# Performance work log

Measured on AMD Instinct MI355X. Metric: run time of the kernel, lower is better.

Reference implementation:

```python
import jax, jax.numpy as jnp
import numpy as np

P_SIZES = (1, 2, 4)
O_SIZE = 32
EPS = 1e-5


def bilin_matrix(S, O):
    """Interpolation matrix (O, S) for torch UpsamplingBilinear2d (align_corners=True)."""
    if S == 1:
        return jnp.ones((O, 1), dtype=jnp.float32)
    pos = jnp.arange(O, dtype=jnp.float32) * ((S - 1) / (O - 1))
    lo = jnp.clip(jnp.floor(pos).astype(jnp.int32), 0, S - 2)
    frac = pos - lo.astype(jnp.float32)
    rows = jnp.arange(O)
    M = jnp.zeros((O, S), dtype=jnp.float32)
    M = M.at[rows, lo].add(1.0 - frac).at[rows, lo + 1].add(frac)
    return M


def setup_inputs() -> dict:
    key = jax.random.key(0)
    ks = jax.random.split(key, 12)
    n, C, H = 16, 512, 32
    c4 = C // 4      # 128, value/pyramid channels
    qk = c4 // 8     # 16, query/key channels inside SAE
    s = 0.05
    return {
        "x": jax.random.normal(ks[0], (n, C, H, H), jnp.float32),
        "rce_w": jax.random.normal(ks[1], (3, c4, C), jnp.float32) * s,   # 1x1 conv per pyramid scale
        "rce_b": jax.random.normal(ks[2], (3, c4), jnp.float32) * s,
        "q_w": jax.random.normal(ks[3], (qk, c4), jnp.float32) * s,       # SAE query 1x1 conv
        "q_b": jax.random.normal(ks[4], (qk,), jnp.float32) * s,
        "k_w": jax.random.normal(ks[5], (qk, c4), jnp.float32) * s,       # SAE key 1x1 conv
        "k_b": jax.random.normal(ks[6], (qk,), jnp.float32) * s,
        "value_w": jax.random.normal(ks[7], (c4, C), jnp.float32) * s,    # value 1x1 conv
        "value_b": jax.random.normal(ks[8], (c4,), jnp.float32) * s,
        "fusion_w": jax.random.normal(ks[9], (C, 3 * c4, 3, 3), jnp.float32) * s,  # 3x3 conv, no bias
        "bn_scale": 1.0 + jax.random.normal(ks[10], (C,), jnp.float32) * s,
        "bn_bias": jax.random.normal(ks[11], (C,), jnp.float32) * s,
        "gamma": jnp.asarray(0.5, jnp.float32),
    }


def reference(x, rce_w, rce_b, q_w, q_b, k_w, k_b, value_w, value_b,
              fusion_w, bn_scale, bn_bias, gamma):
    n, C, H, W = x.shape
    c4 = C // 4
    L = H * W

    # value projection: 1x1 conv then flatten -> (n, c4, L)
    proj_value = (jnp.einsum('oc,nchw->nohw', value_w, x)
                  + value_b[None, :, None, None]).reshape(n, c4, L)

    outs = []
    for i, sz in enumerate(P_SIZES):
        # AdaptiveAvgPool2d((sz, sz)) with divisible input -> exact uniform pooling
        pooled = x.reshape(n, C, sz, H // sz, sz, W // sz).mean(axis=(3, 5))
        # 1x1 conv C -> c4
        feat = jnp.einsum('oc,ncij->noij', rce_w[i], pooled) + rce_b[i][None, :, None, None]
        # bilinear upsample (align_corners=True) to (O_SIZE, O_SIZE)
        M = bilin_matrix(sz, O_SIZE)
        up = jnp.einsum('oi,pj,ncij->ncop', M, M, feat)  # (n, c4, H, W)
        # SAE: query/key 1x1 convs, flatten, bmm + softmax
        q = (jnp.einsum('oc,nchw->nohw', q_w, up) + q_b[None, :, None, None]).reshape(n, -1, L)
        k = (jnp.einsum('oc,nchw->nohw', k_w, up) + k_b[None, :, None, None]).reshape(n, -1, L)
        energy = jnp.einsum('ncl,ncm->nlm', q, k)        # (n, L, L)
        attn = jax.nn.softmax(energy, axis=-1)
        # temp = bmm(value, attn^T): temp[c,m] = sum_l value[c,l] * attn[m,l]
        outs.append(jnp.einsum('ncl,nml->ncm', proj_value, attn).reshape(n, c4, H, W))

    cat = jnp.concatenate(outs, axis=1)                  # (n, 3*c4, H, W)
    y = jax.lax.conv_general_dilated(
        cat, fusion_w, window_strides=(1, 1), padding=((1, 1), (1, 1)),
        dimension_numbers=('NCHW', 'OIHW', 'NCHW'))
    # BatchNorm2d in training mode (default): batch statistics over (N, H, W)
    mean = y.mean(axis=(0, 2, 3))
    var = y.var(axis=(0, 2, 3))
    y = (y - mean[None, :, None, None]) * (bn_scale / jnp.sqrt(var + EPS))[None, :, None, None] \
        + bn_bias[None, :, None, None]
    y = jax.nn.relu(y)
    return gamma * y + x
```

## Files before the change

### kernel.cpp

```cpp
#include <hip/hip_runtime.h>
#include <hip/hip_fp16.h>
#include <math.h>

#define OFF_COR   0u
#define OFF_PVH   2097152u
#define OFF_Y     3145728u
#define OFF_CATP  11534336u
#define OFF_QH    15085568u
#define OFF_KH    15347712u
#define OFF_POOL  16134144u
#define OFF_FEAT  16297984u
#define OFF_AW    16338944u
#define OFF_MEANS 17223680u
#define OFF_STAT  17225728u
#define OFF_VWH   17226752u

typedef __bf16 bf16x8 __attribute__((ext_vector_type(8)));
typedef _Float16 f16x8 __attribute__((ext_vector_type(8)));
typedef _Float16 f16x4 __attribute__((ext_vector_type(4)));
typedef float f32x4 __attribute__((ext_vector_type(4)));

__device__ __forceinline__ unsigned short f2bf(float f) {
  unsigned int u = __float_as_uint(f);
  unsigned int r = u + 0x7fff + ((u >> 16) & 1);
  return (unsigned short)(r >> 16);
}

__device__ __forceinline__ unsigned short f2h(float f) {
  union { _Float16 h; unsigned short u; } cv;
  cv.h = (_Float16)f;
  return cv.u;
}

__device__ __forceinline__ void gload_lds16(const void* g, void* l) {
  __builtin_amdgcn_global_load_lds(
      (const __attribute__((address_space(1))) unsigned int*)g,
      (__attribute__((address_space(3))) unsigned int*)l, 16, 0, 0);
}

__global__ __launch_bounds__(256) void pool_kernel(const float* __restrict__ x,
                                                   float* __restrict__ pool) {
  int b = blockIdx.x;
  int t = threadIdx.x;
  const float4* xp = (const float4*)(x + (size_t)b * 1024);
  float4 v = xp[t];
  float s4 = v.x + v.y + v.z + v.w;
  __shared__ float sm[256];
  __shared__ float p4s[16];
  sm[t] = s4;
  __syncthreads();
  if (t < 16) {
    int br = t >> 2, bc = t & 3;
    float s = 0.f;
#pragma unroll
    for (int rr = 0; rr < 8; ++rr) {
      int base = br * 64 + rr * 8 + bc * 2;
      s += sm[base] + sm[base + 1];
    }
    s *= (1.f / 64.f);
    p4s[t] = s;
    pool[(size_t)b * 20 + t] = s;
  }
  __syncthreads();
  if (t < 4) {
    int i2 = t >> 1, j2 = t & 1;
    float s = (p4s[(2*i2)*4 + 2*j2]     + p4s[(2*i2)*4 + 2*j2 + 1] +
               p4s[(2*i2+1)*4 + 2*j2]   + p4s[(2*i2+1)*4 + 2*j2 + 1]) * 0.25f;
    pool[(size_t)b * 20 + 16 + t] = s;
  }
}

__global__ __launch_bounds__(64) void feat_kernel(const float* __restrict__ pool,
                                                  const float* __restrict__ rce_w,
                                                  const float* __restrict__ rce_b,
                                                  float* __restrict__ feat) {
  int o = blockIdx.x, n = blockIdx.y, t = threadIdx.x;
  float part[20];
#pragma unroll
  for (int j = 0; j < 20; ++j) part[j] = 0.f;
  for (int c = t; c < 512; c += 64) {
    const float* pl = pool + ((size_t)n * 512 + c) * 20;
    float w2 = rce_w[(size_t)(128 + o) * 512 + c];
    float w4 = rce_w[(size_t)(256 + o) * 512 + c];
#pragma unroll
    for (int j = 0; j < 4; ++j)  part[j]     += w2 * pl[16 + j];
#pragma unroll
    for (int j = 0; j < 16; ++j) part[4 + j] += w4 * pl[j];
  }
  __shared__ float red[64][20];
#pragma unroll
  for (int j = 0; j < 20; ++j) red[t][j] = part[j];
  __syncthreads();
  if (t < 20) {
    float s = 0.f;
    for (int i = 0; i < 64; ++i) s += red[i][t];
    s += (t < 4) ? rce_b[128 + o] : rce_b[256 + o];
    feat[((size_t)n * 128 + o) * 20 + t] = s;
  }
}

__global__ __launch_bounds__(256) void qk2_kernel(const float* __restrict__ feat,
                                                  const float* __restrict__ q_w,
                                                  const float* __restrict__ q_b,
                                                  const float* __restrict__ k_w,
                                                  const float* __restrict__ k_b,
                                                  unsigned short* __restrict__ qh,
                                                  unsigned short* __restrict__ kh) {
  int n = blockIdx.x, t = threadIdx.x;
  __shared__ float fL[128 * 20];
  __shared__ float GH[2][16][20];
  for (int idx = t; idx < 2560; idx += 256) fL[idx] = feat[(size_t)n * 2560 + idx];
  __syncthreads();
  for (int idx = t; idx < 640; idx += 256) {
    int which = idx / 320, rem = idx % 320, qc = rem / 20, j = rem % 20;
    const float* w = which ? k_w : q_w;
    float s = which ? k_b[qc] : q_b[qc];
    for (int c = 0; c < 128; ++c) s += w[qc * 128 + c] * fL[c * 20 + j];
    GH[which][qc][j] = s;
  }
  __syncthreads();
  for (int it = blockIdx.y * 2; it < blockIdx.y * 2 + 2; ++it) {
    int row = t + 256 * it;
    int l = row & 1023, which = (row >> 10) & 1, s = row >> 11;
    int ry = l >> 5, cx = l & 31;
    int t0, t1, t2, t3;
    float w0, w1, w2, w3;
    if (s == 0) {
      float a = ry * (1.0f / 31.0f), b = cx * (1.0f / 31.0f);
      t0 = 0; t1 = 1; t2 = 2; t3 = 3;
      w0 = (1.f - a) * (1.f - b); w1 = (1.f - a) * b;
      w2 = a * (1.f - b);         w3 = a * b;
    } else {
      float pr = ry * (3.0f / 31.0f);
      int lr = (int)pr; if (lr > 2) lr = 2;
      float fr = pr - (float)lr;
      float pc = cx * (3.0f / 31.0f);
      int lc = (int)pc; if (lc > 2) lc = 2;
      float fc = pc - (float)lc;
      int base = 4 + lr * 4 + lc;
      t0 = base; t1 = base + 1; t2 = base + 4; t3 = base + 5;
      w0 = (1.f - fr) * (1.f - fc); w1 = (1.f - fr) * fc;
      w2 = fr * (1.f - fc);         w3 = fr * fc;
    }
    float val[16];
#pragma unroll
    for (int qc = 0; qc < 16; ++qc) {
      const float* G = GH[which][qc];
      val[qc] = w0 * G[t0] + w1 * G[t1] + w2 * G[t2] + w3 * G[t3];
    }
    unsigned short* dst = (which ? kh : qh) + (((size_t)(s * 16 + n) * 1024 + l) * 16);
#pragma unroll
    for (int u = 0; u < 4; ++u)
      *(ushort4*)(dst + 4 * u) = make_ushort4(f2h(val[4*u]), f2h(val[4*u+1]),
                                              f2h(val[4*u+2]), f2h(val[4*u+3]));
  }
}

__global__ __launch_bounds__(256) void xcast_kernel(const float* __restrict__ x,
                                                    unsigned short* __restrict__ xT) {
  int lt = blockIdx.x, ct = blockIdx.y, n = blockIdx.z;
  int l0 = lt * 64, c0 = ct * 64, t = threadIdx.x;
  __shared__ float tile[64 * 65];
#pragma unroll
  for (int i = 0; i < 16; ++i) {
    int idx = t + 256 * i;
    int c = idx >> 6, l = idx & 63;
    tile[c * 65 + l] = x[((size_t)n * 512 + c0 + c) * 1024 + l0 + l];
  }
  __syncthreads();
#pragma unroll
  for (int i = 0; i < 16; ++i) {
    int idx = t + 256 * i;
    int l = idx >> 6, c = idx & 63;
    xT[((size_t)n * 1024 + l0 + l) * 512 + c0 + c] = f2h(tile[c * 65 + l]);
  }
}

__global__ __launch_bounds__(256) void vwcast_kernel(const float* __restrict__ vw,
                                                     unsigned short* __restrict__ vwh) {
  int i = blockIdx.x * 256 + threadIdx.x;
  vwh[i] = f2h(vw[i]);
}

__global__ __launch_bounds__(256) void pvmm2_kernel(const unsigned short* __restrict__ vwh,
                                                    const unsigned short* __restrict__ xT,
                                                    const float* __restrict__ vb,
                                                    unsigned short* __restrict__ pvh) {
  int l0 = blockIdx.x * 64;
  int n = blockIdx.y;
  int t = threadIdx.x, lane = t & 63, wv = t >> 6;
  int wm = (wv & 1) * 64, wn = (wv >> 1) * 32;

  __shared__ short Asm[128 * 32];
  __shared__ short Bsm[64 * 32];

  int ar0 = t >> 2,        aq0 = (t & 3) ^ ((ar0 >> 1) & 3);
  int idx1 = t + 256; int ar1 = idx1 >> 2, aq1 = (idx1 & 3) ^ ((ar1 >> 1) & 3);
  int br  = t >> 2,        bq  = (t & 3) ^ ((br >> 1) & 3);
  const unsigned short* Ab0 = vwh + (size_t)ar0 * 512 + aq0 * 8;
  const unsigned short* Ab1 = vwh + (size_t)ar1 * 512 + aq1 * 8;
  const unsigned short* Bb  = xT + ((size_t)n * 1024 + l0 + br) * 512 + bq * 8;
  char* ldsA = (char*)Asm;
  char* ldsB = (char*)Bsm;
  int wvoff = wv * 1024;
  int r15 = lane & 15, kg = lane >> 4;
  int kq = kg ^ ((r15 >> 1) & 3);

  f32x4 acc[4][2];
#pragma unroll
  for (int i = 0; i < 4; ++i)
#pragma unroll
    for (int j = 0; j < 2; ++j) acc[i][j] = (f32x4){0.f, 0.f, 0.f, 0.f};

  for (int k0 = 0; k0 < 512; k0 += 32) {
    __syncthreads();
    gload_lds16(Ab0 + k0, ldsA + wvoff);
    gload_lds16(Ab1 + k0, ldsA + 4096 + wvoff);
    gload_lds16(Bb + k0,  ldsB + wvoff);
    __syncthreads();
    f16x8 af[4], bfr[2];
#pragma unroll
    for (int mt2 = 0; mt2 < 4; ++mt2)
      af[mt2] = *(const f16x8*)&Asm[(wm + mt2 * 16 + r15) * 32 + kq * 8];
#pragma unroll
    for (int nt2 = 0; nt2 < 2; ++nt2)
      bfr[nt2] = *(const f16x8*)&Bsm[(wn + nt2 * 16 + r15) * 32 + kq * 8];
#pragma unroll
    for (int mt2 = 0; mt2 < 4; ++mt2)
#pragma unroll
      for (int nt2 = 0; nt2 < 2; ++nt2)
        acc[mt2][nt2] = __builtin_amdgcn_mfma_f32_16x16x32_f16(af[mt2], bfr[nt2], acc[mt2][nt2], 0, 0, 0);
  }

  int c_lo = wm + (lane >> 4) * 4;
  int l_lo = wn + (lane & 15);
#pragma unroll
  for (int mt2 = 0; mt2 < 4; ++mt2)
#pragma unroll
    for (int nt2 = 0; nt2 < 2; ++nt2) {
      int l = l0 + l_lo + nt2 * 16;
#pragma unroll
      for (int r = 0; r < 4; ++r) {
        int c = c_lo + mt2 * 16 + r;
        pvh[((size_t)n * 128 + c) * 1024 + l] = f2h(acc[mt2][nt2][r] + vb[c]);
      }
    }
}

__global__ __launch_bounds__(256) void mean_kernel(const unsigned short* __restrict__ pvh,
                                                   float* __restrict__ means) {
  int c = blockIdx.x, n = blockIdx.y, t = threadIdx.x;
  f16x4 v = ((const f16x4*)(pvh + ((size_t)n * 128 + c) * 1024))[t];
  float s = (float)v[0] + (float)v[1] + (float)v[2] + (float)v[3];
  for (int o = 32; o > 0; o >>= 1) s += __shfl_down(s, o);
  __shared__ float wsum[4];
  if ((t & 63) == 0) wsum[t >> 6] = s;
  __syncthreads();
  if (t == 0) means[n * 128 + c] = (wsum[0] + wsum[1] + wsum[2] + wsum[3]) * (1.f / 1024.f);
}

__global__ __launch_bounds__(64) void basecor_kernel(const float* __restrict__ means,
                                                     const float* __restrict__ fw,
                                                     float* __restrict__ cor) {
  int oc = blockIdx.x, n = blockIdx.y, t = threadIdx.x;
  float S[9];
#pragma unroll
  for (int j = 0; j < 9; ++j) S[j] = 0.f;
  for (int c = t; c < 128; c += 64) {
    float m = means[n * 128 + c];
    const float* wp = fw + (size_t)oc * 3456 + c * 9;
#pragma unroll
    for (int j = 0; j < 9; ++j) S[j] += m * wp[j];
  }
  __shared__ float red[64][9];
  __shared__ float Sf[9];
#pragma unroll
  for (int j = 0; j < 9; ++j) red[t][j] = S[j];
  __syncthreads();
  if (t < 9) {
    float s = 0.f;
    for (int i = 0; i < 64; ++i) s += red[i][t];
    Sf[t] = s;
  }
  __syncthreads();
  if (t < 9) {
    int a = t / 3, b = t % 3;
    float s = 0.f;
#pragma unroll
    for (int ky = 0; ky < 3; ++ky) {
      if ((a == 0 && ky == 0) || (a == 2 && ky == 2)) continue;
#pragma unroll
      for (int kx = 0; kx < 3; ++kx) {
        if ((b == 0 && kx == 0) || (b == 2 && kx == 2)) continue;
        s += Sf[ky * 3 + kx];
      }
    }
    cor[((size_t)n * 512 + oc) * 9 + t] = s;
  }
}

__global__ __launch_bounds__(128) void fillcat_kernel(unsigned short* __restrict__ catp) {
  int b = blockIdx.x;
  int n = b / 132, e = b % 132;
  int py, px;
  if (e < 34)       { py = 0;          px = e; }
  else if (e < 68)  { py = 33;         px = e - 34; }
  else if (e < 100) { py = e - 68 + 1; px = 0; }
  else              { py = e - 100 + 1; px = 33; }
  unsigned int* row = (unsigned int*)(catp + ((size_t)n * 1156 + py * 34 + px) * 256);
  row[threadIdx.x] = 0u;
}

__global__ __launch_bounds__(256) void wcast_kernel(const float* __restrict__ fw,
                                                    unsigned short* __restrict__ Aw) {
  int oc = blockIdx.x, t = threadIdx.x;
  for (int j = t; j < 2304; j += 256) {
    int seg = j >> 8, ic2 = j & 255;
    Aw[(size_t)oc * 2304 + j] = f2bf(fw[(size_t)oc * 3456 + (128 + ic2) * 9 + seg]);
  }
}

__global__ __launch_bounds__(256) void fattn_kernel(const unsigned short* __restrict__ qh,
                                                    const unsigned short* __restrict__ kh,
                                                    const unsigned short* __restrict__ pvh,
                                                    unsigned short* __restrict__ catp) {
  int m0 = blockIdx.x * 64;
  int n = blockIdx.y, sc = blockIdx.z;
  int t = threadIdx.x, lane = t & 63, wv = t >> 6;
  int wc = (wv >> 1) * 64;
  int wm2 = (wv & 1) * 32;
  int r15 = lane & 15, kg = lane >> 4;
  int kq = kg ^ ((r15 >> 1) & 3);

  const unsigned short* qb  = qh + ((size_t)(sc * 16 + n) * 1024 + m0 + wv * 16) * 16;
  const unsigned short* kb  = kh + ((size_t)(sc * 16 + n) * 1024) * 16;
  const unsigned short* pvb = pvh + (size_t)n * 128 * 1024;

  __shared__ short PVs[2 * 2 * 128 * 32];
  __shared__ _Float16 Us[64 * 72];
  __shared__ float rsum[64];

  f16x8 zf = {0, 0, 0, 0, 0, 0, 0, 0};
  f16x8 qa = (kg < 2) ? *(const f16x8*)(qb + r15 * 16 + kg * 8) : zf;

  int prow = t >> 2;
  int aq = (t & 3) ^ ((prow >> 1) & 3);
  const unsigned short* Pb0 = pvb + (size_t)prow * 1024 + aq * 8;
  const unsigned short* Pb1 = pvb + (size_t)(prow + 64) * 1024 + aq * 8;
  char* ldsPV = (char*)PVs;
  int wvoff = wv * 1024;

  f32x4 acc[4][2];
#pragma unroll
  for (int i = 0; i < 4; ++i)
#pragma unroll
    for (int j = 0; j < 2; ++j) acc[i][j] = (f32x4){0.f, 0.f, 0.f, 0.f};
  float rs[4] = {0.f, 0.f, 0.f, 0.f};

  gload_lds16(Pb0,      ldsPV + wvoff);
  gload_lds16(Pb1,      ldsPV + 4096 + wvoff);
  gload_lds16(Pb0 + 32, ldsPV + 8192 + wvoff);
  gload_lds16(Pb1 + 32, ldsPV + 12288 + wvoff);

  for (int it = 0; it < 16; ++it) {
    int cur = it & 1;
    int l0 = it * 64;
    f16x8 kbf[4];
#pragma unroll
    for (int lt = 0; lt < 4; ++lt)
      kbf[lt] = (kg < 2)
        ? *(const f16x8*)(kb + (size_t)(l0 + lt * 16 + r15) * 16 + kg * 8) : zf;
    if (it < 15) {
      char* dst = ldsPV + (cur ^ 1) * 16384 + wvoff;
      gload_lds16(Pb0 + l0 + 64, dst);
      gload_lds16(Pb1 + l0 + 64, dst + 4096);
      gload_lds16(Pb0 + l0 + 96, dst + 8192);
      gload_lds16(Pb1 + l0 + 96, dst + 12288);
    }
    f32x4 sacc[4];
#pragma unroll
    for (int lt = 0; lt < 4; ++lt)
      sacc[lt] = __builtin_amdgcn_mfma_f32_16x16x32_f16(qa, kbf[lt], (f32x4){0.f,0.f,0.f,0.f}, 0, 0, 0);
#pragma unroll
    for (int lt = 0; lt < 4; ++lt)
#pragma unroll
      for (int r = 0; r < 4; ++r) {
        float e = __expf(sacc[lt][r]);
        Us[(wv * 16 + kg * 4 + r) * 72 + lt * 16 + r15] = (_Float16)e;
        rs[r] += e;
      }
    asm volatile("s_waitcnt vmcnt(4) lgkmcnt(0)" ::: "memory");
    __builtin_amdgcn_s_barrier();
    __builtin_amdgcn_sched_barrier(0);
#pragma unroll
    for (int ks = 0; ks < 2; ++ks) {
      f16x8 bfr[2];
#pragma unroll
      for (int nt = 0; nt < 2; ++nt)
        bfr[nt] = *(const f16x8*)&Us[(wm2 + nt * 16 + r15) * 72 + ks * 32 + kg * 8];
#pragma unroll
      for (int ct = 0; ct < 4; ++ct) {
        f16x8 af = *(const f16x8*)&PVs[cur * 8192 + ks * 4096 + (wc + ct * 16 + r15) * 32 + kq * 8];
#pragma unroll
        for (int nt = 0; nt < 2; ++nt)
          acc[ct][nt] = __builtin_amdgcn_mfma_f32_16x16x32_f16(af, bfr[nt], acc[ct][nt], 0, 0, 0);
      }
    }
    asm volatile("s_waitcnt lgkmcnt(0)" ::: "memory");
    __builtin_amdgcn_s_barrier();
    __builtin_amdgcn_sched_barrier(0);
  }

#pragma unroll
  for (int r = 0; r < 4; ++r) {
    rs[r] += __shfl_xor(rs[r], 1);
    rs[r] += __shfl_xor(rs[r], 2);
    rs[r] += __shfl_xor(rs[r], 4);
    rs[r] += __shfl_xor(rs[r], 8);
  }
  if (r15 == 0) {
#pragma unroll
    for (int r = 0; r < 4; ++r) rsum[wv * 16 + kg * 4 + r] = rs[r];
  }
  __syncthreads();

#pragma unroll
  for (int nt = 0; nt < 2; ++nt) {
    float inv = 1.f / rsum[wm2 + nt * 16 + r15];
    int pix = m0 + wm2 + nt * 16 + r15;
    unsigned short* ob = catp + ((size_t)n * 1156 + ((pix >> 5) + 1) * 34 + (pix & 31) + 1) * 256
                       + sc * 128 + wc + kg * 4;
#pragma unroll
    for (int ct = 0; ct < 4; ++ct) {
      ushort4 o = make_ushort4(f2bf(acc[ct][nt][0] * inv), f2bf(acc[ct][nt][1] * inv),
                               f2bf(acc[ct][nt][2] * inv), f2bf(acc[ct][nt][3] * inv));
      *(ushort4*)(ob + ct * 16) = o;
    }
  }
}

__device__ __forceinline__ void conv_stage(const unsigned short* __restrict__ Aw,
                                           const unsigned short* __restrict__ catp,
                                           size_t abase0, size_t abase1,
                                           size_t bbase0, size_t bbase1,
                                           int s, char* la, char* lb, int wvoff) {
  int seg = s >> 2;
  size_t akk  = (size_t)s * 64;
  size_t boff = (size_t)((seg / 3) * 34 + (seg % 3)) * 256 + (size_t)(s & 3) * 64;
  gload_lds16(Aw + abase0 + akk,          la + wvoff);
  gload_lds16(Aw + abase1 + akk,          la + 4096 + wvoff);
  gload_lds16(Aw + abase0 + akk + 32,     la + 8192 + wvoff);
  gload_lds16(Aw + abase1 + akk + 32,     la + 12288 + wvoff);
  gload_lds16(catp + bbase0 + boff,       lb + wvoff);
  gload_lds16(catp + bbase1 + boff,       lb + 4096 + wvoff);
  gload_lds16(catp + bbase0 + boff + 32,  lb + 8192 + wvoff);
  gload_lds16(catp + bbase1 + boff + 32,  lb + 12288 + wvoff);
}

__device__ __forceinline__ void conv_comp(const short* As_, const short* Bs_,
                                          int wm, int wn, int r15, int kq,
                                          f32x4 acc[4][4]) {
  bf16x8 af[4], bf[4];
#pragma unroll
  for (int mt = 0; mt < 4; ++mt)
    af[mt] = *(const bf16x8*)&As_[(wm + mt * 16 + r15) * 32 + kq * 8];
#pragma unroll
  for (int nt = 0; nt < 4; ++nt)
    bf[nt] = *(const bf16x8*)&Bs_[(wn + nt * 16 + r15) * 32 + kq * 8];
#pragma unroll
  for (int mt = 0; mt < 4; ++mt)
#pragma unroll
    for (int nt = 0; nt < 4; ++nt)
      acc[mt][nt] = __builtin_amdgcn_mfma_f32_16x16x32_bf16(af[mt], bf[nt], acc[mt][nt], 0, 0, 0);
}

__global__ __launch_bounds__(256) void convmm_kernel(const unsigned short* __restrict__ Aw,
                                                     const unsigned short* __restrict__ catp,
                                                     const float* __restrict__ cor,
                                                     float* __restrict__ y) {
  int ntile = blockIdx.x;
  int n = ntile >> 3, y0 = (ntile & 7) * 4;
  int m0 = blockIdx.y * 128;
  int t = threadIdx.x;
  int lane = t & 63, wv = t >> 6;
  int wm = (wv & 1) * 64, wn = (wv >> 1) * 64;

  __shared__ short Asm[2 * 2 * 128 * 32];
  __shared__ short Bsm[2 * 2 * 128 * 32];

  int idx0 = t, idx1 = t + 256;
  int ar0 = idx0 >> 2, aq0 = (idx0 & 3) ^ ((ar0 >> 1) & 3);
  int ar1 = idx1 >> 2, aq1 = (idx1 & 3) ^ ((ar1 >> 1) & 3);
  size_t abase0 = (size_t)(m0 + ar0) * 2304 + aq0 * 8;
  size_t abase1 = (size_t)(m0 + ar1) * 2304 + aq1 * 8;
  size_t bbase0 = ((size_t)n * 1156 + (size_t)(y0 + (ar0 >> 5)) * 34 + (ar0 & 31)) * 256 + aq0 * 8;
  size_t bbase1 = ((size_t)n * 1156 + (size_t)(y0 + (ar1 >> 5)) * 34 + (ar1 & 31)) * 256 + aq1 * 8;
  char* ldsA = (char*)Asm;
  char* ldsB = (char*)Bsm;
  int wvoff = wv * 1024;

  int r15 = lane & 15, kg = lane >> 4;
  int kq = kg ^ ((r15 >> 1) & 3);

  f32x4 acc[4][4];
#pragma unroll
  for (int i = 0; i < 4; ++i)
#pragma unroll
    for (int j = 0; j < 4; ++j) acc[i][j] = (f32x4){0.f, 0.f, 0.f, 0.f};

  conv_stage(Aw, catp, abase0, abase1, bbase0, bbase1, 0, ldsA, ldsB, wvoff);
  __syncthreads();

#pragma unroll 2
  for (int s = 0; s < 36; ++s) {
    char* la = ldsA + (s & 1) * 16384;
    char* lb = ldsB + (s & 1) * 16384;
    if (s < 35)
      conv_stage(Aw, catp, abase0, abase1, bbase0, bbase1, s + 1,
                 ldsA + ((s + 1) & 1) * 16384, ldsB + ((s + 1) & 1) * 16384, wvoff);
    conv_comp((const short*)la,          (const short*)lb,          wm, wn, r15, kq, acc);
    conv_comp((const short*)(la + 8192), (const short*)(lb + 8192), wm, wn, r15, kq, acc);
    __syncthreads();
  }

  int pixbase = (ntile & 7) * 128 + wn + (lane & 15);
  int ocbase = m0 + wm + (lane >> 4) * 4;
#pragma unroll
  for (int mt = 0; mt < 4; ++mt)
#pragma unroll
    for (int nt = 0; nt < 4; ++nt) {
      int oc = ocbase + mt * 16;
      int pix = pixbase + nt * 16;
      int py = pix >> 5, px = pix & 31;
      int yc = (py == 0) ? 0 : ((py == 31) ? 2 : 1);
      int xc = (px == 0) ? 0 : ((px == 31) ? 2 : 1);
      const float* cp = cor + ((size_t)n * 512 + oc) * 9 + yc * 3 + xc;
      float* yp = y + ((size_t)n * 512 + oc) * 1024 + pix;
#pragma unroll
      for (int r = 0; r < 4; ++r) yp[(size_t)r * 1024] = acc[mt][nt][r] + cp[(size_t)r * 9];
    }
}

__global__ __launch_bounds__(256) void bnstat_kernel(const float* __restrict__ y,
                                                     const float* __restrict__ bn_scale,
                                                     const float* __restrict__ bn_bias,
                                                     float* __restrict__ stats) {
  int oc = blockIdx.x, t = threadIdx.x;
  float s = 0.f, ss = 0.f;
  for (int n = 0; n < 16; ++n) {
    float4 v = ((const float4*)(y + ((size_t)n * 512 + oc) * 1024))[t];
    s  += v.x + v.y + v.z + v.w;
    ss += v.x * v.x + v.y * v.y + v.z * v.z + v.w * v.w;
  }
  for (int o = 32; o > 0; o >>= 1) {
    s  += __shfl_down(s, o);
    ss += __shfl_down(ss, o);
  }
  __shared__ float rs[4], rss[4];
  if ((t & 63) == 0) { rs[t >> 6] = s; rss[t >> 6] = ss; }
  __syncthreads();
  if (t == 0) {
    float S = rs[0] + rs[1] + rs[2] + rs[3];
    float SS = rss[0] + rss[1] + rss[2] + rss[3];
    float mean = S * (1.f / 16384.f);
    float var = SS * (1.f / 16384.f) - mean * mean;
    float se = bn_scale[oc] / sqrtf(var + 1e-5f);
    stats[oc * 2] = se;
    stats[oc * 2 + 1] = bn_bias[oc] - mean * se;
  }
}

__global__ __launch_bounds__(256) void final_kernel(const float* __restrict__ y,
                                                    const float* __restrict__ x,
                                                    const float* __restrict__ stats,
                                                    const float* __restrict__ gamma,
                                                    float* __restrict__ outp) {
  int b = blockIdx.x;
  int c = b & 511;
  int t = threadIdx.x;
  float se = stats[c * 2], sh = stats[c * 2 + 1], g = gamma[0];
  float4 yv = ((const float4*)(y + (size_t)b * 1024))[t];
  float4 xv = ((const float4*)(x + (size_t)b * 1024))[t];
  float4 o;
  o.x = g * fmaxf(yv.x * se + sh, 0.f) + xv.x;
  o.y = g * fmaxf(yv.y * se + sh, 0.f) + xv.y;
  o.z = g * fmaxf(yv.z * se + sh, 0.f) + xv.z;
  o.w = g * fmaxf(yv.w * se + sh, 0.f) + xv.w;
  ((float4*)(outp + (size_t)b * 1024))[t] = o;
}

extern "C" void kernel_launch(void* const* d_in, const int* in_sizes, int n_in,
                              void* d_out, int out_size, void* d_ws, size_t ws_size,
                              hipStream_t stream) {
  const float* x        = (const float*)d_in[0];
  const float* rce_w    = (const float*)d_in[1];
  const float* rce_b    = (const float*)d_in[2];
  const float* q_w      = (const float*)d_in[3];
  const float* q_b      = (const float*)d_in[4];
  const float* k_w      = (const float*)d_in[5];
  const float* k_b      = (const float*)d_in[6];
  const float* value_w  = (const float*)d_in[7];
  const float* value_b  = (const float*)d_in[8];
  const float* fw       = (const float*)d_in[9];
  const float* bn_scale = (const float*)d_in[10];
  const float* bn_bias  = (const float*)d_in[11];
  const float* gamma    = (const float*)d_in[12];

  float* ws    = (float*)d_ws;
  float* cor   = ws + OFF_COR;
  unsigned short* pvh = (unsigned short*)(ws + OFF_PVH);
  float* ybuf  = ws + OFF_Y;
  unsigned short* xTbuf = (unsigned short*)(ws + OFF_Y);
  unsigned short* catp = (unsigned short*)(ws + OFF_CATP);
  unsigned short* qh   = (unsigned short*)(ws + OFF_QH);
  unsigned short* kh   = (unsigned short*)(ws + OFF_KH);
  float* pool  = ws + OFF_POOL;
  float* feat  = ws + OFF_FEAT;
  unsigned short* Aw = (unsigned short*)(ws + OFF_AW);
  float* means = ws + OFF_MEANS;
  float* stats = ws + OFF_STAT;
  unsigned short* vwh = (unsigned short*)(ws + OFF_VWH);
  float* outp  = (float*)d_out;

  hipLaunchKernelGGL(pool_kernel,    dim3(8192),       dim3(256), 0, stream, x, pool);
  hipLaunchKernelGGL(feat_kernel,    dim3(128, 16),    dim3(64),  0, stream, pool, rce_w, rce_b, feat);
  hipLaunchKernelGGL(qk2_kernel,     dim3(16, 8),      dim3(256), 0, stream, feat, q_w, q_b, k_w, k_b, qh, kh);
  hipLaunchKernelGGL(xcast_kernel,   dim3(16, 8, 16),  dim3(256), 0, stream, x, xTbuf);
  hipLaunchKernelGGL(vwcast_kernel,  dim3(256),        dim3(256), 0, stream, value_w, vwh);
  hipLaunchKernelGGL(pvmm2_kernel,   dim3(16, 16),     dim3(256), 0, stream, vwh, xTbuf, value_b, pvh);
  hipLaunchKernelGGL(mean_kernel,    dim3(128, 16),    dim3(256), 0, stream, pvh, means);
  hipLaunchKernelGGL(basecor_kernel, dim3(512, 16),    dim3(64),  0, stream, means, fw, cor);
  hipLaunchKernelGGL(fillcat_kernel, dim3(2112),       dim3(128), 0, stream, catp);
  hipLaunchKernelGGL(wcast_kernel,   dim3(512),        dim3(256), 0, stream, fw, Aw);
  hipLaunchKernelGGL(fattn_kernel,   dim3(16, 16, 2),  dim3(256), 0, stream, qh, kh, pvh, catp);
  hipLaunchKernelGGL(convmm_kernel,  dim3(128, 4),     dim3(256), 0, stream, Aw, catp, cor, ybuf);
  hipLaunchKernelGGL(bnstat_kernel,  dim3(512),        dim3(256), 0, stream, ybuf, bn_scale, bn_bias, stats);
  hipLaunchKernelGGL(final_kernel,   dim3(8192),       dim3(256), 0, stream, ybuf, x, stats, gamma, outp);
}
```

Baseline: 244.6 us.

## Double-buffer pvmm2 K loop and merge weight-cast/pad-fill kernels into one

```diff
diff --git a/kernel.cpp b/kernel.cpp
--- a/kernel.cpp
+++ b/kernel.cpp
@@ -176,10 +176,32 @@
   }
 }
 
-__global__ __launch_bounds__(256) void vwcast_kernel(const float* __restrict__ vw,
-                                                     unsigned short* __restrict__ vwh) {
-  int i = blockIdx.x * 256 + threadIdx.x;
-  vwh[i] = f2h(vw[i]);
+__global__ __launch_bounds__(256) void prep_kernel(const float* __restrict__ fw,
+                                                   const float* __restrict__ vw,
+                                                   unsigned short* __restrict__ Aw,
+                                                   unsigned short* __restrict__ vwh,
+                                                   unsigned short* __restrict__ catp) {
+  int b = blockIdx.x, t = threadIdx.x;
+  if (b < 512) {
+    int oc = b;
+    for (int j = t; j < 2304; j += 256) {
+      int seg = j >> 8, ic2 = j & 255;
+      Aw[(size_t)oc * 2304 + j] = f2bf(fw[(size_t)oc * 3456 + (128 + ic2) * 9 + seg]);
+    }
+  } else if (b < 768) {
+    int i = (b - 512) * 256 + t;
+    vwh[i] = f2h(vw[i]);
+  } else {
+    int e = (b - 768) * 2 + (t >> 7);
+    int n = e / 132, r = e % 132;
+    int py, px;
+    if (r < 34)       { py = 0;           px = r; }
+    else if (r < 68)  { py = 33;          px = r - 34; }
+    else if (r < 100) { py = r - 68 + 1;  px = 0; }
+    else              { py = r - 100 + 1; px = 33; }
+    unsigned int* row = (unsigned int*)(catp + ((size_t)n * 1156 + py * 34 + px) * 256);
+    row[t & 127] = 0u;
+  }
 }
 
 __global__ __launch_bounds__(256) void pvmm2_kernel(const unsigned short* __restrict__ vwh,
@@ -191,8 +213,8 @@
   int t = threadIdx.x, lane = t & 63, wv = t >> 6;
   int wm = (wv & 1) * 64, wn = (wv >> 1) * 32;
 
-  __shared__ short Asm[128 * 32];
-  __shared__ short Bsm[64 * 32];
+  __shared__ short Asm[2 * 2 * 128 * 32];
+  __shared__ short Bsm[2 * 2 * 64 * 32];
 
   int ar0 = t >> 2,        aq0 = (t & 3) ^ ((ar0 >> 1) & 3);
   int idx1 = t + 256; int ar1 = idx1 >> 2, aq1 = (idx1 & 3) ^ ((ar1 >> 1) & 3);
@@ -212,25 +234,45 @@
 #pragma unroll
     for (int j = 0; j < 2; ++j) acc[i][j] = (f32x4){0.f, 0.f, 0.f, 0.f};
 
-  for (int k0 = 0; k0 < 512; k0 += 32) {
+#define PV_STAGE(s, la, lb) do {                          \
+    int k0_ = (s) * 64;                                   \
+    gload_lds16(Ab0 + k0_,      (la) + wvoff);            \
+    gload_lds16(Ab1 + k0_,      (la) + 4096 + wvoff);     \
+    gload_lds16(Ab0 + k0_ + 32, (la) + 8192 + wvoff);     \
+    gload_lds16(Ab1 + k0_ + 32, (la) + 12288 + wvoff);    \
+    gload_lds16(Bb + k0_,       (lb) + wvoff);            \
+    gload_lds16(Bb + k0_ + 32,  (lb) + 4096 + wvoff);     \
+  } while (0)
+
+  PV_STAGE(0, ldsA, ldsB);
+  __syncthreads();
+
+#pragma unroll 2
+  for (int s = 0; s < 8; ++s) {
+    char* la = ldsA + (s & 1) * 16384;
+    char* lb = ldsB + (s & 1) * 8192;
+    if (s < 7)
+      PV_STAGE(s + 1, ldsA + ((s + 1) & 1) * 16384, ldsB + ((s + 1) & 1) * 8192);
+#pragma unroll
+    for (int c = 0; c < 2; ++c) {
+      const short* As_ = (const short*)(la + c * 8192);
+      const short* Bs_ = (const short*)(lb + c * 4096);
+      f16x8 af[4], bfr[2];
+#pragma unroll
+      for (int mt2 = 0; mt2 < 4; ++mt2)
+        af[mt2] = *(const f16x8*)&As_[(wm + mt2 * 16 + r15) * 32 + kq * 8];
+#pragma unroll
+      for (int nt2 = 0; nt2 < 2; ++nt2)
+        bfr[nt2] = *(const f16x8*)&Bs_[(wn + nt2 * 16 + r15) * 32 + kq * 8];
+#pragma unroll
+      for (int mt2 = 0; mt2 < 4; ++mt2)
+#pragma unroll
+        for (int nt2 = 0; nt2 < 2; ++nt2)
+          acc[mt2][nt2] = __builtin_amdgcn_mfma_f32_16x16x32_f16(af[mt2], bfr[nt2], acc[mt2][nt2], 0, 0, 0);
+    }
     __syncthreads();
-    gload_lds16(Ab0 + k0, ldsA + wvoff);
-    gload_lds16(Ab1 + k0, ldsA + 4096 + wvoff);
-    gload_lds16(Bb + k0,  ldsB + wvoff);
-    __syncthreads();
-    f16x8 af[4], bfr[2];
-#pragma unroll
-    for (int mt2 = 0; mt2 < 4; ++mt2)
-      af[mt2] = *(const f16x8*)&Asm[(wm + mt2 * 16 + r15) * 32 + kq * 8];
-#pragma unroll
-    for (int nt2 = 0; nt2 < 2; ++nt2)
-      bfr[nt2] = *(const f16x8*)&Bsm[(wn + nt2 * 16 + r15) * 32 + kq * 8];
-#pragma unroll
-    for (int mt2 = 0; mt2 < 4; ++mt2)
-#pragma unroll
-      for (int nt2 = 0; nt2 < 2; ++nt2)
-        acc[mt2][nt2] = __builtin_amdgcn_mfma_f32_16x16x32_f16(af[mt2], bfr[nt2], acc[mt2][nt2], 0, 0, 0);
-  }
+  }
+#undef PV_STAGE
 
   int c_lo = wm + (lane >> 4) * 4;
   int l_lo = wn + (lane & 15);
@@ -296,27 +338,6 @@
       }
     }
     cor[((size_t)n * 512 + oc) * 9 + t] = s;
-  }
-}
-
-__global__ __launch_bounds__(128) void fillcat_kernel(unsigned short* __restrict__ catp) {
-  int b = blockIdx.x;
-  int n = b / 132, e = b % 132;
-  int py, px;
-  if (e < 34)       { py = 0;          px = e; }
-  else if (e < 68)  { py = 33;         px = e - 34; }
-  else if (e < 100) { py = e - 68 + 1; px = 0; }
-  else              { py = e - 100 + 1; px = 33; }
-  unsigned int* row = (unsigned int*)(catp + ((size_t)n * 1156 + py * 34 + px) * 256);
-  row[threadIdx.x] = 0u;
-}
-
-__global__ __launch_bounds__(256) void wcast_kernel(const float* __restrict__ fw,
-                                                    unsigned short* __restrict__ Aw) {
-  int oc = blockIdx.x, t = threadIdx.x;
-  for (int j = t; j < 2304; j += 256) {
-    int seg = j >> 8, ic2 = j & 255;
-    Aw[(size_t)oc * 2304 + j] = f2bf(fw[(size_t)oc * 3456 + (128 + ic2) * 9 + seg]);
   }
 }
 
@@ -626,12 +647,10 @@
   hipLaunchKernelGGL(feat_kernel,    dim3(128, 16),    dim3(64),  0, stream, pool, rce_w, rce_b, feat);
   hipLaunchKernelGGL(qk2_kernel,     dim3(16, 8),      dim3(256), 0, stream, feat, q_w, q_b, k_w, k_b, qh, kh);
   hipLaunchKernelGGL(xcast_kernel,   dim3(16, 8, 16),  dim3(256), 0, stream, x, xTbuf);
-  hipLaunchKernelGGL(vwcast_kernel,  dim3(256),        dim3(256), 0, stream, value_w, vwh);
+  hipLaunchKernelGGL(prep_kernel,    dim3(1824),       dim3(256), 0, stream, fw, value_w, Aw, vwh, catp);
   hipLaunchKernelGGL(pvmm2_kernel,   dim3(16, 16),     dim3(256), 0, stream, vwh, xTbuf, value_b, pvh);
   hipLaunchKernelGGL(mean_kernel,    dim3(128, 16),    dim3(256), 0, stream, pvh, means);
   hipLaunchKernelGGL(basecor_kernel, dim3(512, 16),    dim3(64),  0, stream, means, fw, cor);
-  hipLaunchKernelGGL(fillcat_kernel, dim3(2112),       dim3(128), 0, stream, catp);
-  hipLaunchKernelGGL(wcast_kernel,   dim3(512),        dim3(256), 0, stream, fw, Aw);
   hipLaunchKernelGGL(fattn_kernel,   dim3(16, 16, 2),  dim3(256), 0, stream, qh, kh, pvh, catp);
   hipLaunchKernelGGL(convmm_kernel,  dim3(128, 4),     dim3(256), 0, stream, Aw, catp, cor, ybuf);
   hipLaunchKernelGGL(bnstat_kernel,  dim3(512),        dim3(256), 0, stream, ybuf, bn_scale, bn_bias, stats);
```

New measurement: 243.3 us. About the same (-0.5%).
